# Kernel tuning notes

Hardware: AMD Instinct MI355X
Metric: run time of the kernel (lower is better)

The kernel has to match this reference:

```python
import jax, jax.numpy as jnp
import numpy as np

TOP_K = 8

def setup_inputs() -> dict:
    key = jax.random.key(0)
    k1, k2, k3 = jax.random.split(key, 3)
    B, S, D, R, N = 4, 2048, 1024, 128, 64
    x = jax.random.normal(k1, (B, S, D), dtype=jnp.float32)
    router_w = jax.random.normal(k2, (N, D), dtype=jnp.float32) * (1.0 / np.sqrt(D))
    compress_neurons = jax.random.normal(k3, (N, D, R), dtype=jnp.float32) * (1.0 / np.sqrt(D))
    return {"x": x, "router_w": router_w, "compress_neurons": compress_neurons}

def reference(x, router_w, compress_neurons):
    # x: [B,S,D]; router_w: [N,D]; compress_neurons: [N,D,R]
    scores = jnp.einsum('bsd,nd->bsn', x, router_w)                 # [B,S,N]
    topk_scores, topk_idx = jax.lax.top_k(scores, TOP_K)            # [B,S,K]
    weights = jax.nn.softmax(topk_scores, axis=-1)                  # [B,S,K]
    # Project through ALL neurons then gather top-k (avoids materializing
    # the [B,S,K,D,R] expanded weight tensor; math identical to gather-then-einsum).
    proj_all = jnp.einsum('bsd,ndr->bsnr', x, compress_neurons)     # [B,S,N,R]
    proj = jnp.take_along_axis(proj_all, topk_idx[..., None], axis=2)  # [B,S,K,R]
    output = jnp.einsum('bskr,bsk->bsr', proj, weights)             # [B,S,R]
    return output, weights, topk_idx, scores
```

## Files before the change

kernel.cpp:

```cpp
#include <hip/hip_runtime.h>
#include <math.h>

typedef unsigned int  u32;
typedef unsigned short u16;
typedef unsigned long long u64;

#define T_TOK 8192
#define DDIM  1024
#define RDIM  128
#define NEXP  64
#define TOPK  8
#define NENT  (T_TOK * TOPK)
#define NCHUNK 256

#define OUT_O_OFF 0
#define OUT_W_OFF (T_TOK * RDIM)
#define OUT_I_OFF (OUT_W_OFF + T_TOK * TOPK)
#define OUT_S_OFF (OUT_I_OFF + T_TOK * TOPK)


typedef __attribute__((ext_vector_type(8))) short bf16x8;
typedef __attribute__((ext_vector_type(4))) float f32x4;

__device__ __forceinline__ u16 f2bf(float f) {
  union { float f; u32 u; } v; v.f = f;
  u32 r = v.u + 0x7fffu + ((v.u >> 16) & 1u);
  return (u16)(r >> 16);
}
__device__ __forceinline__ float bf2f(u16 h) {
  union { u32 u; float f; } v; v.u = ((u32)h) << 16;
  return v.f;
}

#define GL_LDS(gp, lp) __builtin_amdgcn_global_load_lds( \
    (const __attribute__((address_space(1))) void*)(gp), \
    (__attribute__((address_space(3))) void*)(lp), 16, 0, 0)

__global__ __launch_bounds__(256) void convert_x_kernel(
    const float* __restrict__ x, u16* __restrict__ xbf)
{
  const int i = blockIdx.x * 256 + threadIdx.x;
  const float4 a = reinterpret_cast<const float4*>(x)[i * 2];
  const float4 b = reinterpret_cast<const float4*>(x)[i * 2 + 1];
  uint4 o;
  o.x = (u32)f2bf(a.x) | ((u32)f2bf(a.y) << 16);
  o.y = (u32)f2bf(a.z) | ((u32)f2bf(a.w) << 16);
  o.z = (u32)f2bf(b.x) | ((u32)f2bf(b.y) << 16);
  o.w = (u32)f2bf(b.z) | ((u32)f2bf(b.w) << 16);
  reinterpret_cast<uint4*>(xbf)[i] = o;
}

__global__ __launch_bounds__(256) void convert_cn_kernel(
    const float* __restrict__ cn, u16* __restrict__ cnbt)
{
  const int n  = blockIdx.x;
  const int d0 = blockIdx.y * 32;
  const int r0 = blockIdx.z * 32;
  __shared__ float ts[32][33];
  const int t = threadIdx.x;
  {
    const int dr = t >> 3, rq = t & 7;
    float4 v = *reinterpret_cast<const float4*>(
        cn + ((size_t)n * DDIM + d0 + dr) * RDIM + r0 + rq * 4);
    ts[dr][rq * 4 + 0] = v.x; ts[dr][rq * 4 + 1] = v.y;
    ts[dr][rq * 4 + 2] = v.z; ts[dr][rq * 4 + 3] = v.w;
  }
  __syncthreads();
  {
    const int rr = t >> 3, dq = t & 7;
    ushort4 o;
    o.x = f2bf(ts[dq * 4 + 0][rr]);
    o.y = f2bf(ts[dq * 4 + 1][rr]);
    o.z = f2bf(ts[dq * 4 + 2][rr]);
    o.w = f2bf(ts[dq * 4 + 3][rr]);
    *reinterpret_cast<ushort4*>(
        cnbt + ((size_t)n * RDIM + r0 + rr) * DDIM + d0 + dq * 4) = o;
  }
}

__global__ __launch_bounds__(256) void router_part_kernel(
    const float* __restrict__ x, const float* __restrict__ rw,
    double* __restrict__ partials, u16* __restrict__ xbf, int dlen)
{
  __shared__ double xs[32][38];
  __shared__ double wsd[64][38];

  const int tok0  = blockIdx.x * 32;
  const int slice = blockIdx.y;
  const int d0    = slice * dlen;
  const int t     = threadIdx.x;
  const int ti    = t & 15;
  const int ei    = t >> 4;

  const int srow = t >> 3;
  const int sq   = t & 7;
  const int dd   = sq * 4;

  double acc[2][4];
#pragma unroll
  for (int a = 0; a < 2; ++a)
#pragma unroll
    for (int b = 0; b < 4; ++b) acc[a][b] = 0.0;

  for (int dc = d0; dc < d0 + dlen; dc += 32) {
    {
      float4 v = *reinterpret_cast<const float4*>(
          x + (size_t)(tok0 + srow) * DDIM + dc + dd);
      double2 p0; p0.x = (double)v.x; p0.y = (double)v.y;
      double2 p1; p1.x = (double)v.z; p1.y = (double)v.w;
      *reinterpret_cast<double2*>(&xs[srow][dd])     = p0;
      *reinterpret_cast<double2*>(&xs[srow][dd + 2]) = p1;
      ushort4 o;
      o.x = f2bf(v.x); o.y = f2bf(v.y); o.z = f2bf(v.z); o.w = f2bf(v.w);
      *reinterpret_cast<ushort4*>(
          xbf + (size_t)(tok0 + srow) * DDIM + dc + dd) = o;
    }
#pragma unroll
    for (int i = 0; i < 2; ++i) {
      const int row = srow + i * 32;
      float4 wv = *reinterpret_cast<const float4*>(
          rw + (size_t)row * DDIM + dc + dd);
      double2 q0; q0.x = (double)wv.x; q0.y = (double)wv.y;
      double2 q1; q1.x = (double)wv.z; q1.y = (double)wv.w;
      *reinterpret_cast<double2*>(&wsd[row][dd])     = q0;
      *reinterpret_cast<double2*>(&wsd[row][dd + 2]) = q1;
    }
    __syncthreads();

#pragma unroll 4
    for (int d2 = 0; d2 < 32; d2 += 2) {
      double2 xv0 = *reinterpret_cast<const double2*>(&xs[ti +  0][d2]);
      double2 xv1 = *reinterpret_cast<const double2*>(&xs[ti + 16][d2]);
      double2 wv0 = *reinterpret_cast<const double2*>(&wsd[ei +  0][d2]);
      double2 wv1 = *reinterpret_cast<const double2*>(&wsd[ei + 16][d2]);
      double2 wv2 = *reinterpret_cast<const double2*>(&wsd[ei + 32][d2]);
      double2 wv3 = *reinterpret_cast<const double2*>(&wsd[ei + 48][d2]);
      acc[0][0] += xv0.x * wv0.x; acc[0][0] += xv0.y * wv0.y;
      acc[0][1] += xv0.x * wv1.x; acc[0][1] += xv0.y * wv1.y;
      acc[0][2] += xv0.x * wv2.x; acc[0][2] += xv0.y * wv2.y;
      acc[0][3] += xv0.x * wv3.x; acc[0][3] += xv0.y * wv3.y;
      acc[1][0] += xv1.x * wv0.x; acc[1][0] += xv1.y * wv0.y;
      acc[1][1] += xv1.x * wv1.x; acc[1][1] += xv1.y * wv1.y;
      acc[1][2] += xv1.x * wv2.x; acc[1][2] += xv1.y * wv2.y;
      acc[1][3] += xv1.x * wv3.x; acc[1][3] += xv1.y * wv3.y;
    }
    __syncthreads();
  }

#pragma unroll
  for (int jt = 0; jt < 2; ++jt)
#pragma unroll
    for (int je = 0; je < 4; ++je)
      partials[((size_t)slice * T_TOK + tok0 + ti + 16 * jt) * NEXP
               + ei + 16 * je] = acc[jt][je];
}

__global__ __launch_bounds__(256) void router_gemm_kernel(
    const float* __restrict__ x, const float* __restrict__ rw,
    float* __restrict__ out)
{
  __shared__ float xs[32][68];
  __shared__ float wsm[64][68];
  const int tok0 = blockIdx.x * 32;
  const int t  = threadIdx.x;
  const int ti2 = (t & 15) * 2;
  const int e4  = (t >> 4) * 4;

  double acc[2][4];
#pragma unroll
  for (int a = 0; a < 2; ++a)
#pragma unroll
    for (int b = 0; b < 4; ++b) acc[a][b] = 0.0;

  for (int dc = 0; dc < DDIM; dc += 64) {
#pragma unroll
    for (int p = 0; p < 2; ++p) {
      const int idx = t + p * 256;
      const int row = idx >> 4, q = idx & 15;
      float4 v = *reinterpret_cast<const float4*>(
          x + (size_t)(tok0 + row) * DDIM + dc + q * 4);
      *reinterpret_cast<float4*>(&xs[row][q * 4]) = v;
    }
#pragma unroll
    for (int p = 0; p < 4; ++p) {
      const int idx = t + p * 256;
      const int row = idx >> 4, q = idx & 15;
      float4 v = *reinterpret_cast<const float4*>(
          rw + (size_t)row * DDIM + dc + q * 4);
      *reinterpret_cast<float4*>(&wsm[row][q * 4]) = v;
    }
    __syncthreads();

#pragma unroll 2
    for (int d4 = 0; d4 < 64; d4 += 4) {
      float4 xv0 = *reinterpret_cast<const float4*>(&xs[ti2][d4]);
      float4 xv1 = *reinterpret_cast<const float4*>(&xs[ti2 + 1][d4]);
      float4 wv0 = *reinterpret_cast<const float4*>(&wsm[e4 + 0][d4]);
      float4 wv1 = *reinterpret_cast<const float4*>(&wsm[e4 + 1][d4]);
      float4 wv2 = *reinterpret_cast<const float4*>(&wsm[e4 + 2][d4]);
      float4 wv3 = *reinterpret_cast<const float4*>(&wsm[e4 + 3][d4]);
      acc[0][0] += (double)xv0.x * (double)wv0.x; acc[0][0] += (double)xv0.y * (double)wv0.y;
      acc[0][0] += (double)xv0.z * (double)wv0.z; acc[0][0] += (double)xv0.w * (double)wv0.w;
      acc[0][1] += (double)xv0.x * (double)wv1.x; acc[0][1] += (double)xv0.y * (double)wv1.y;
      acc[0][1] += (double)xv0.z * (double)wv1.z; acc[0][1] += (double)xv0.w * (double)wv1.w;
      acc[0][2] += (double)xv0.x * (double)wv2.x; acc[0][2] += (double)xv0.y * (double)wv2.y;
      acc[0][2] += (double)xv0.z * (double)wv2.z; acc[0][2] += (double)xv0.w * (double)wv2.w;
      acc[0][3] += (double)xv0.x * (double)wv3.x; acc[0][3] += (double)xv0.y * (double)wv3.y;
      acc[0][3] += (double)xv0.z * (double)wv3.z; acc[0][3] += (double)xv0.w * (double)wv3.w;
      acc[1][0] += (double)xv1.x * (double)wv0.x; acc[1][0] += (double)xv1.y * (double)wv0.y;
      acc[1][0] += (double)xv1.z * (double)wv0.z; acc[1][0] += (double)xv1.w * (double)wv0.w;
      acc[1][1] += (double)xv1.x * (double)wv1.x; acc[1][1] += (double)xv1.y * (double)wv1.y;
      acc[1][1] += (double)xv1.z * (double)wv1.z; acc[1][1] += (double)xv1.w * (double)wv1.w;
      acc[1][2] += (double)xv1.x * (double)wv2.x; acc[1][2] += (double)xv1.y * (double)wv2.y;
      acc[1][2] += (double)xv1.z * (double)wv2.z; acc[1][2] += (double)xv1.w * (double)wv2.w;
      acc[1][3] += (double)xv1.x * (double)wv3.x; acc[1][3] += (double)xv1.y * (double)wv3.y;
      acc[1][3] += (double)xv1.z * (double)wv3.z; acc[1][3] += (double)xv1.w * (double)wv3.w;
    }
    __syncthreads();
  }

#pragma unroll
  for (int a = 0; a < 2; ++a) {
    float4 o;
    o.x = (float)acc[a][0]; o.y = (float)acc[a][1];
    o.z = (float)acc[a][2]; o.w = (float)acc[a][3];
    *reinterpret_cast<float4*>(
        out + OUT_S_OFF + (size_t)(tok0 + ti2 + a) * NEXP + e4) = o;
  }
}

__global__ __launch_bounds__(256) void topk_kernel(
    const double* __restrict__ partials,
    float* __restrict__ out, int* __restrict__ idx_int, int nslice)
{
  const int token = blockIdx.x * 4 + (threadIdx.x >> 6);
  const int lane  = threadIdx.x & 63;

  float v;
  if (nslice > 0) {
    double s = 0.0;
    for (int sl = 0; sl < nslice; ++sl)
      s += partials[((size_t)sl * T_TOK + token) * NEXP + lane];
    v = (float)s;
    out[OUT_S_OFF + (size_t)token * NEXP + lane] = v;
  } else {
    v = out[OUT_S_OFF + (size_t)token * NEXP + lane];
  }

  float cur = v;
  float topv[TOPK];
  int   topi[TOPK];
  for (int k = 0; k < TOPK; ++k) {
    float bv = cur;
    int   bi = lane;
#pragma unroll
    for (int off = 32; off >= 1; off >>= 1) {
      float ov = __shfl_xor(bv, off);
      int   oi = __shfl_xor(bi, off);
      if (ov > bv || (ov == bv && oi < bi)) { bv = ov; bi = oi; }
    }
    topv[k] = bv;
    topi[k] = bi;
    if (lane == bi) cur = -INFINITY;
  }
  const float m = topv[0];
  float wk[TOPK];
  float s = 0.f;
#pragma unroll
  for (int k = 0; k < TOPK; ++k) { wk[k] = expf(topv[k] - m); s += wk[k]; }
  const float inv = 1.f / s;

  if (lane < TOPK) {
    out[OUT_W_OFF + (size_t)token * TOPK + lane] = wk[lane] * inv;
    out[OUT_I_OFF + (size_t)token * TOPK + lane] = (float)topi[lane];
    idx_int[(size_t)token * TOPK + lane] = topi[lane];
  }
}

__global__ __launch_bounds__(256) void hist_kernel(
    const int* __restrict__ idx_int, int* __restrict__ histT)
{
  const int chunk = blockIdx.x;
  const int t = threadIdx.x;
  const int w = t >> 6, l = t & 63;
  const int v = idx_int[chunk * 256 + t];

  __shared__ int wh[4][64];
  int cnt = 0;
#pragma unroll 8
  for (int s = 0; s < NEXP; ++s) {
    const u64 b = __ballot(v == s);
    if (l == s) cnt = (int)__popcll(b);
  }
  wh[w][l] = cnt;
  __syncthreads();
  if (t < NEXP)
    histT[t * NCHUNK + chunk] = wh[0][t] + wh[1][t] + wh[2][t] + wh[3][t];
}

__global__ __launch_bounds__(256) void offsets_kernel(
    const int* __restrict__ histT, int* __restrict__ chunk_off,
    int* __restrict__ counts, int* __restrict__ offsets)
{
  const int n = blockIdx.x;
  const int t = threadIdx.x;
  const int w = t >> 6, l = t & 63;
  __shared__ int bsum[4];
  __shared__ int wsum[4];

  int part = 0;
  for (int i = t; i < n * NCHUNK; i += 256) part += histT[i];
#pragma unroll
  for (int off = 32; off >= 1; off >>= 1) part += __shfl_xor(part, off);
  if (l == 0) bsum[w] = part;
  __syncthreads();
  const int base = bsum[0] + bsum[1] + bsum[2] + bsum[3];

  const int h = histT[n * NCHUNK + t];
  int s = h;
#pragma unroll
  for (int off = 1; off < 64; off <<= 1) {
    const int o = __shfl_up(s, off);
    if (l >= off) s += o;
  }
  if (l == 63) wsum[w] = s;
  __syncthreads();
  int wpre = 0;
#pragma unroll
  for (int w2 = 0; w2 < 4; ++w2) if (w2 < w) wpre += wsum[w2];
  const int incl = s + wpre;

  chunk_off[n * NCHUNK + t] = base + incl - h;
  if (t == 255) counts[n] = incl;
  if (t == 0)   offsets[n] = base;
}

__global__ __launch_bounds__(256) void scatter_kernel(
    const int* __restrict__ idx_int, const int* __restrict__ chunk_off,
    int* __restrict__ list_tk)
{
  const int chunk = blockIdx.x;
  const int t = threadIdx.x;
  const int w = t >> 6, l = t & 63;
  const int e = chunk * 256 + t;
  const int v = idx_int[e];

  __shared__ int wh[4][64];
  int myrank = 0, cnt = 0;
#pragma unroll 8
  for (int s = 0; s < NEXP; ++s) {
    const u64 b = __ballot(v == s);
    if (v == s) myrank = (int)__popcll(b & ((1ull << l) - 1ull));
    if (l == s) cnt = (int)__popcll(b);
  }
  wh[w][l] = cnt;
  __syncthreads();
  int pre = 0;
#pragma unroll
  for (int w2 = 0; w2 < 4; ++w2) if (w2 < w) pre += wh[w2][v];
  list_tk[chunk_off[v * NCHUNK + chunk] + pre + myrank] = e;
}

template<int MODE>
__global__ __launch_bounds__(256) void mfma_gemm_kernel(
    const u16* __restrict__ xbf, const u16* __restrict__ cnbt,
    const int* __restrict__ counts, const int* __restrict__ offsets,
    const int* __restrict__ list_tk,
    float* __restrict__ out, u16* __restrict__ projbf)
{
  const int n = blockIdx.x;
  const int cnt = counts[n];
  const int start = blockIdx.y * 64;
  if (start >= cnt) return;
  const int nrows = min(64, cnt - start);
  const int base = offsets[n] + start;

  __shared__ __align__(16) u16 smem[2 * 12288];

  const int t  = threadIdx.x;
  const int l  = t & 63;
  const int w  = t >> 6;
  const int cl = l & 15;
  const int kq = l >> 4;

  const int rsub = l >> 3;
  const int p8   = ((l & 7) ^ rsub) * 8;

  int toki[2];
#pragma unroll
  for (int i = 0; i < 2; ++i) {
    const int r = w * 16 + i * 8 + rsub;
    toki[i] = list_tk[base + min(r, nrows - 1)] >> 3;
  }
  const u16* cnb = cnbt + (size_t)n * RDIM * DDIM;

  f32x4 acc[8];
#pragma unroll
  for (int f = 0; f < 8; ++f) acc[f] = (f32x4){0.f, 0.f, 0.f, 0.f};

#pragma unroll
  for (int i = 0; i < 2; ++i) {
    const int rs = w * 16 + i * 8;
    GL_LDS(xbf + (size_t)toki[i] * DDIM + p8, smem + rs * 64);
  }
#pragma unroll
  for (int i = 0; i < 4; ++i) {
    const int rs = w * 32 + i * 8;
    GL_LDS(cnb + (size_t)(rs + rsub) * DDIM + p8, smem + 4096 + rs * 64);
  }

  int cur = 0;
  for (int c = 0; c < 16; ++c) {
    if (c < 15) {
      const int dc = (c + 1) * 64;
      const int po = (cur ^ 1) * 12288;
#pragma unroll
      for (int i = 0; i < 2; ++i) {
        const int rs = w * 16 + i * 8;
        GL_LDS(xbf + (size_t)toki[i] * DDIM + dc + p8, smem + po + rs * 64);
      }
#pragma unroll
      for (int i = 0; i < 4; ++i) {
        const int rs = w * 32 + i * 8;
        GL_LDS(cnb + (size_t)(rs + rsub) * DDIM + dc + p8,
               smem + po + 4096 + rs * 64);
      }
      asm volatile("s_waitcnt vmcnt(6)" ::: "memory");
    } else {
      asm volatile("s_waitcnt vmcnt(0)" ::: "memory");
    }
    __builtin_amdgcn_s_barrier();
    __builtin_amdgcn_sched_barrier(0);

    const u16* A = smem + cur * 12288;
    const u16* B = A + 4096;
    __builtin_amdgcn_s_setprio(1);
#pragma unroll
    for (int ks = 0; ks < 2; ++ks) {
      const int piece = ks * 4 + kq;
      const int ar = w * 16 + cl;
      bf16x8 a = *reinterpret_cast<const bf16x8*>(
          &A[ar * 64 + ((piece ^ (ar & 7)) * 8)]);
#pragma unroll
      for (int f = 0; f < 8; ++f) {
        const int br = f * 16 + cl;
        bf16x8 b = *reinterpret_cast<const bf16x8*>(
            &B[br * 64 + ((piece ^ (br & 7)) * 8)]);
        acc[f] = __builtin_amdgcn_mfma_f32_16x16x32_bf16(a, b, acc[f], 0, 0, 0);
      }
    }
    __builtin_amdgcn_s_setprio(0);
    asm volatile("s_waitcnt lgkmcnt(0)" ::: "memory");
    __builtin_amdgcn_s_barrier();
    cur ^= 1;
  }

#pragma unroll
  for (int j = 0; j < 4; ++j) {
    const int row = w * 16 + kq * 4 + j;
    if (row < nrows) {
      const int tk = list_tk[base + row];
      if (MODE == 0) {
        u16* prow = projbf + (size_t)tk * RDIM + cl;
#pragma unroll
        for (int f = 0; f < 8; ++f) prow[f * 16] = f2bf(acc[f][j]);
      } else {
        const float wg = out[OUT_W_OFF + tk];
        float* orow = out + OUT_O_OFF + (size_t)(tk >> 3) * RDIM + cl;
#pragma unroll
        for (int f = 0; f < 8; ++f) unsafeAtomicAdd(&orow[f * 16], wg * acc[f][j]);
      }
    }
  }
}

__global__ __launch_bounds__(256) void combine_kernel(
    const u16* __restrict__ projbf, float* __restrict__ out)
{
  const int token = blockIdx.x * 4 + (threadIdx.x >> 6);
  const int l = threadIdx.x & 63;
  float wts[TOPK];
#pragma unroll
  for (int k = 0; k < TOPK; ++k) wts[k] = out[OUT_W_OFF + (size_t)token * TOPK + k];
  float s0 = 0.f, s1 = 0.f;
#pragma unroll
  for (int k = 0; k < TOPK; ++k) {
    const u32 u = *reinterpret_cast<const u32*>(
        projbf + ((size_t)token * TOPK + k) * RDIM + l * 2);
    s0 += wts[k] * bf2f((u16)(u & 0xffff));
    s1 += wts[k] * bf2f((u16)(u >> 16));
  }
  float2 o; o.x = s0; o.y = s1;
  *reinterpret_cast<float2*>(out + OUT_O_OFF + (size_t)token * RDIM + l * 2) = o;
}

__global__ __launch_bounds__(256) void gemm_f32_kernel(
    const float* __restrict__ x, const float* __restrict__ cn,
    const int* __restrict__ counts, const int* __restrict__ offsets,
    const int* __restrict__ list_tk, float* __restrict__ out)
{
  const int n = blockIdx.x;
  const int cnt = counts[n];
  const int start = blockIdx.y * 64;
  if (start >= cnt) return;
  const int nrows = min(64, cnt - start);
  const int base = offsets[n] + start;

  __shared__ float xs[64][33];
  __shared__ float cs[32][RDIM];

  const int t  = threadIdx.x;
  const int tg = t & 31;
  const int rc = t >> 5;
  const int row0 = tg * 2, row1 = tg * 2 + 1;
  const int rA = t >> 3, rB = rA + 32, jA = t & 7;
  const int tokA = (rA < nrows) ? (list_tk[base + rA] >> 3) : -1;
  const int tokB = (rB < nrows) ? (list_tk[base + rB] >> 3) : -1;

  float acc0[16], acc1[16];
#pragma unroll
  for (int j = 0; j < 16; ++j) { acc0[j] = 0.f; acc1[j] = 0.f; }
  const float* cbase = cn + (size_t)n * DDIM * RDIM;

  for (int dc = 0; dc < DDIM; dc += 32) {
    {
      float4 v = make_float4(0.f, 0.f, 0.f, 0.f);
      if (tokA >= 0) v = *reinterpret_cast<const float4*>(x + (size_t)tokA * DDIM + dc + jA * 4);
      xs[rA][jA * 4 + 0] = v.x; xs[rA][jA * 4 + 1] = v.y;
      xs[rA][jA * 4 + 2] = v.z; xs[rA][jA * 4 + 3] = v.w;
      float4 u = make_float4(0.f, 0.f, 0.f, 0.f);
      if (tokB >= 0) u = *reinterpret_cast<const float4*>(x + (size_t)tokB * DDIM + dc + jA * 4);
      xs[rB][jA * 4 + 0] = u.x; xs[rB][jA * 4 + 1] = u.y;
      xs[rB][jA * 4 + 2] = u.z; xs[rB][jA * 4 + 3] = u.w;
    }
#pragma unroll
    for (int p = 0; p < 4; ++p) {
      const int f = t + p * 256;
      const int dr = f >> 5, c4 = f & 31;
      float4 v = *reinterpret_cast<const float4*>(cbase + (size_t)(dc + dr) * RDIM + c4 * 4);
      *reinterpret_cast<float4*>(&cs[dr][c4 * 4]) = v;
    }
    __syncthreads();
#pragma unroll 4
    for (int d = 0; d < 32; ++d) {
      const float x0 = xs[row0][d];
      const float x1 = xs[row1][d];
      const float4* cp = reinterpret_cast<const float4*>(&cs[d][rc * 16]);
      float cv[16];
      *reinterpret_cast<float4*>(&cv[0])  = cp[0];
      *reinterpret_cast<float4*>(&cv[4])  = cp[1];
      *reinterpret_cast<float4*>(&cv[8])  = cp[2];
      *reinterpret_cast<float4*>(&cv[12]) = cp[3];
#pragma unroll
      for (int j = 0; j < 16; ++j) { acc0[j] += x0 * cv[j]; acc1[j] += x1 * cv[j]; }
    }
    __syncthreads();
  }
  if (row0 < nrows) {
    const int tk = list_tk[base + row0];
    const float wg = out[OUT_W_OFF + tk];
    float* orow = out + OUT_O_OFF + (size_t)(tk >> 3) * RDIM + rc * 16;
#pragma unroll
    for (int j = 0; j < 16; ++j) unsafeAtomicAdd(&orow[j], acc0[j] * wg);
  }
  if (row1 < nrows) {
    const int tk = list_tk[base + row1];
    const float wg = out[OUT_W_OFF + tk];
    float* orow = out + OUT_O_OFF + (size_t)(tk >> 3) * RDIM + rc * 16;
#pragma unroll
    for (int j = 0; j < 16; ++j) unsafeAtomicAdd(&orow[j], acc1[j] * wg);
  }
}

extern "C" void kernel_launch(void* const* d_in, const int* in_sizes, int n_in,
                              void* d_out, int out_size, void* d_ws, size_t ws_size,
                              hipStream_t stream)
{
  (void)in_sizes; (void)n_in; (void)out_size;

  const float* x  = (const float*)d_in[0];
  const float* rw = (const float*)d_in[1];
  const float* cn = (const float*)d_in[2];
  float* out = (float*)d_out;

  char* wsb = (char*)d_ws;
  int* counts    = (int*)(wsb);
  int* offsets   = (int*)(wsb + 256);
  int* list_tk   = (int*)(wsb + 1024);
  int* idx_int   = (int*)(wsb + 263168);
  int* histT     = (int*)(wsb + 525312);
  int* chunk_off = (int*)(wsb + 590848);

  const size_t OFF_XBF  = 656384;
  const size_t SZ_XBF   = (size_t)T_TOK * DDIM * 2;
  const size_t SZ_CNBT  = (size_t)NEXP * RDIM * DDIM * 2;
  const size_t SZ_PROJ  = (size_t)T_TOK * TOPK * RDIM * 2;
  const size_t OFF_PART = OFF_XBF + SZ_XBF + SZ_CNBT + SZ_PROJ;
  u16* xbf    = (u16*)(wsb + OFF_XBF);
  u16* cnbt   = (u16*)(wsb + OFF_XBF + SZ_XBF);
  u16* projbf = (u16*)(wsb + OFF_XBF + SZ_XBF + SZ_CNBT);
  double* partials = (double*)(wsb + OFF_PART);

  const int tier = (ws_size >= OFF_PART) ? 0
                 : (ws_size >= OFF_XBF + SZ_XBF + SZ_CNBT) ? 1 : 2;

  const size_t slice_bytes = (size_t)T_TOK * NEXP * sizeof(double);
  int nslice = 0;
  if (tier == 0 && ws_size >= OFF_PART + 4 * slice_bytes) nslice = 4;

  if (tier != 0)
    hipMemsetAsync(d_out, 0, (size_t)T_TOK * RDIM * sizeof(float), stream);

  if (tier <= 1) {
    if (nslice == 0)
      convert_x_kernel<<<4096, 256, 0, stream>>>(x, xbf);
    convert_cn_kernel<<<dim3(NEXP, 32, 4), 256, 0, stream>>>(cn, cnbt);
  }

  if (nslice > 0) {
    router_part_kernel<<<dim3(T_TOK / 32, nslice), 256, 0, stream>>>(
        x, rw, partials, xbf, DDIM / nslice);
    topk_kernel<<<T_TOK / 4, 256, 0, stream>>>(partials, out, idx_int, nslice);
  } else {
    router_gemm_kernel<<<T_TOK / 32, 256, 0, stream>>>(x, rw, out);
    topk_kernel<<<T_TOK / 4, 256, 0, stream>>>(partials, out, idx_int, 0);
  }

  hist_kernel<<<NCHUNK, 256, 0, stream>>>(idx_int, histT);
  offsets_kernel<<<NEXP, 256, 0, stream>>>(histT, chunk_off, counts, offsets);
  scatter_kernel<<<NCHUNK, 256, 0, stream>>>(idx_int, chunk_off, list_tk);

  if (tier == 0) {
    dim3 grid(NEXP, 128);
    mfma_gemm_kernel<0><<<grid, 256, 0, stream>>>(xbf, cnbt, counts, offsets, list_tk, out, projbf);
    combine_kernel<<<T_TOK / 4, 256, 0, stream>>>(projbf, out);
  } else if (tier == 1) {
    dim3 grid(NEXP, 128);
    mfma_gemm_kernel<1><<<grid, 256, 0, stream>>>(xbf, cnbt, counts, offsets, list_tk, out, projbf);
  } else {
    dim3 grid(NEXP, 128);
    gemm_f32_kernel<<<grid, 256, 0, stream>>>(x, cn, counts, offsets, list_tk, out);
  }
}
```

Before: 122.5 us.

## Enlarge router partial-GEMM token tile to 128 and split D into 8 slices

```diff
diff --git a/kernel.cpp b/kernel.cpp
--- a/kernel.cpp
+++ b/kernel.cpp
@@ -82,73 +82,74 @@
     const float* __restrict__ x, const float* __restrict__ rw,
     double* __restrict__ partials, u16* __restrict__ xbf, int dlen)
 {
-  __shared__ double xs[32][38];
+  __shared__ double xs[128][38];
   __shared__ double wsd[64][38];
 
-  const int tok0  = blockIdx.x * 32;
+  const int tok0  = blockIdx.x * 128;
   const int slice = blockIdx.y;
   const int d0    = slice * dlen;
   const int t     = threadIdx.x;
   const int ti    = t & 15;
   const int ei    = t >> 4;
 
-  const int srow = t >> 3;
-  const int sq   = t & 7;
-  const int dd   = sq * 4;
-
-  double acc[2][4];
-#pragma unroll
-  for (int a = 0; a < 2; ++a)
+  const int xrow = t >> 1;
+  const int xq   = (t & 1) * 16;
+  const int wrow = t >> 2;
+  const int wq   = (t & 3) * 8;
+
+  double acc[8][4];
+#pragma unroll
+  for (int a = 0; a < 8; ++a)
 #pragma unroll
     for (int b = 0; b < 4; ++b) acc[a][b] = 0.0;
 
   for (int dc = d0; dc < d0 + dlen; dc += 32) {
-    {
+#pragma unroll
+    for (int i = 0; i < 4; ++i) {
+      const int dd = xq + i * 4;
       float4 v = *reinterpret_cast<const float4*>(
-          x + (size_t)(tok0 + srow) * DDIM + dc + dd);
+          x + (size_t)(tok0 + xrow) * DDIM + dc + dd);
       double2 p0; p0.x = (double)v.x; p0.y = (double)v.y;
       double2 p1; p1.x = (double)v.z; p1.y = (double)v.w;
-      *reinterpret_cast<double2*>(&xs[srow][dd])     = p0;
-      *reinterpret_cast<double2*>(&xs[srow][dd + 2]) = p1;
+      *reinterpret_cast<double2*>(&xs[xrow][dd])     = p0;
+      *reinterpret_cast<double2*>(&xs[xrow][dd + 2]) = p1;
       ushort4 o;
       o.x = f2bf(v.x); o.y = f2bf(v.y); o.z = f2bf(v.z); o.w = f2bf(v.w);
       *reinterpret_cast<ushort4*>(
-          xbf + (size_t)(tok0 + srow) * DDIM + dc + dd) = o;
+          xbf + (size_t)(tok0 + xrow) * DDIM + dc + dd) = o;
     }
 #pragma unroll
     for (int i = 0; i < 2; ++i) {
-      const int row = srow + i * 32;
+      const int dd = wq + i * 4;
       float4 wv = *reinterpret_cast<const float4*>(
-          rw + (size_t)row * DDIM + dc + dd);
+          rw + (size_t)wrow * DDIM + dc + dd);
       double2 q0; q0.x = (double)wv.x; q0.y = (double)wv.y;
       double2 q1; q1.x = (double)wv.z; q1.y = (double)wv.w;
-      *reinterpret_cast<double2*>(&wsd[row][dd])     = q0;
-      *reinterpret_cast<double2*>(&wsd[row][dd + 2]) = q1;
+      *reinterpret_cast<double2*>(&wsd[wrow][dd])     = q0;
+      *reinterpret_cast<double2*>(&wsd[wrow][dd + 2]) = q1;
     }
     __syncthreads();
 
-#pragma unroll 4
+#pragma unroll 2
     for (int d2 = 0; d2 < 32; d2 += 2) {
-      double2 xv0 = *reinterpret_cast<const double2*>(&xs[ti +  0][d2]);
-      double2 xv1 = *reinterpret_cast<const double2*>(&xs[ti + 16][d2]);
       double2 wv0 = *reinterpret_cast<const double2*>(&wsd[ei +  0][d2]);
       double2 wv1 = *reinterpret_cast<const double2*>(&wsd[ei + 16][d2]);
       double2 wv2 = *reinterpret_cast<const double2*>(&wsd[ei + 32][d2]);
       double2 wv3 = *reinterpret_cast<const double2*>(&wsd[ei + 48][d2]);
-      acc[0][0] += xv0.x * wv0.x; acc[0][0] += xv0.y * wv0.y;
-      acc[0][1] += xv0.x * wv1.x; acc[0][1] += xv0.y * wv1.y;
-      acc[0][2] += xv0.x * wv2.x; acc[0][2] += xv0.y * wv2.y;
-      acc[0][3] += xv0.x * wv3.x; acc[0][3] += xv0.y * wv3.y;
-      acc[1][0] += xv1.x * wv0.x; acc[1][0] += xv1.y * wv0.y;
-      acc[1][1] += xv1.x * wv1.x; acc[1][1] += xv1.y * wv1.y;
-      acc[1][2] += xv1.x * wv2.x; acc[1][2] += xv1.y * wv2.y;
-      acc[1][3] += xv1.x * wv3.x; acc[1][3] += xv1.y * wv3.y;
+#pragma unroll
+      for (int j = 0; j < 8; ++j) {
+        double2 xv = *reinterpret_cast<const double2*>(&xs[ti + 16 * j][d2]);
+        acc[j][0] += xv.x * wv0.x; acc[j][0] += xv.y * wv0.y;
+        acc[j][1] += xv.x * wv1.x; acc[j][1] += xv.y * wv1.y;
+        acc[j][2] += xv.x * wv2.x; acc[j][2] += xv.y * wv2.y;
+        acc[j][3] += xv.x * wv3.x; acc[j][3] += xv.y * wv3.y;
+      }
     }
     __syncthreads();
   }
 
 #pragma unroll
-  for (int jt = 0; jt < 2; ++jt)
+  for (int jt = 0; jt < 8; ++jt)
 #pragma unroll
     for (int je = 0; je < 4; ++je)
       partials[((size_t)slice * T_TOK + tok0 + ti + 16 * jt) * NEXP
@@ -606,7 +607,8 @@
 
   const size_t slice_bytes = (size_t)T_TOK * NEXP * sizeof(double);
   int nslice = 0;
-  if (tier == 0 && ws_size >= OFF_PART + 4 * slice_bytes) nslice = 4;
+  if (tier == 0 && ws_size >= OFF_PART + 8 * slice_bytes) nslice = 8;
+  else if (tier == 0 && ws_size >= OFF_PART + 4 * slice_bytes) nslice = 4;
 
   if (tier != 0)
     hipMemsetAsync(d_out, 0, (size_t)T_TOK * RDIM * sizeof(float), stream);
@@ -618,7 +620,7 @@
   }
 
   if (nslice > 0) {
-    router_part_kernel<<<dim3(T_TOK / 32, nslice), 256, 0, stream>>>(
+    router_part_kernel<<<dim3(T_TOK / 128, nslice), 256, 0, stream>>>(
         x, rw, partials, xbf, DDIM / nslice);
     topk_kernel<<<T_TOK / 4, 256, 0, stream>>>(partials, out, idx_int, nslice);
   } else {
```

Measured after the change: 121.8 us. About the same (-0.6%).
